# Optimization experiments

Measured on AMD Instinct MI355X. Metric: run time of the kernel, lower is better.

## Reference

```python
import jax, jax.numpy as jnp
import numpy as np

T, M, L, NL, NH, FF = 4096, 512, 128, 2, 8, 2048
NI, NO = 256, 32

def _ln(x, g, b, eps=1e-5):
    mu = x.mean(-1, keepdims=True)
    var = ((x - mu) ** 2).mean(-1, keepdims=True)
    return (x - mu) * jax.lax.rsqrt(var + eps) * g + b

def _mha(x, Wqkv, bqkv, Wo, bo, nh):
    t, m = x.shape
    hd = m // nh
    qkv = x @ Wqkv.T + bqkv  # (T, 3M)
    q, k, v = jnp.split(qkv, 3, axis=-1)
    q = q.reshape(t, nh, hd).transpose(1, 0, 2)
    k = k.reshape(t, nh, hd).transpose(1, 0, 2)
    v = v.reshape(t, nh, hd).transpose(1, 0, 2)
    scores = jnp.einsum('htd,hsd->hts', q, k) / jnp.sqrt(jnp.float32(hd))
    attn = jax.nn.softmax(scores, axis=-1)
    o = jnp.einsum('hts,hsd->htd', attn, v).transpose(1, 0, 2).reshape(t, m)
    return o @ Wo.T + bo

def _seg_softmax(a, seg, n):
    m = jax.lax.stop_gradient(jax.ops.segment_max(a, seg, num_segments=n))
    e = jnp.exp(a - m[seg])
    s = jax.ops.segment_sum(e, seg, num_segments=n)
    return e / s[seg]

def _conv1d(x, K, b, pad):
    y = jax.lax.conv_general_dilated(x, K, (1,), [pad], dimension_numbers=('NCH', 'OIH', 'NCH'))
    return y + b[None, :, None]

def _bn_eval(x, g, b, eps=1e-5):
    # eval-mode BatchNorm1d, running_mean=0, running_var=1
    scale = g * jax.lax.rsqrt(jnp.float32(1.0) + eps)
    if x.ndim == 3:
        return x * scale[None, :, None] + b[None, :, None]
    return x * scale + b

def setup_inputs() -> dict:
    key = jax.random.key(0)
    ks = iter(jax.random.split(key, 64))
    r = lambda shape: jax.random.normal(next(ks), shape, jnp.float32) * 0.02
    datas = jax.random.normal(next(ks), (T, M), jnp.float32)
    Seq_ids = jnp.repeat(jnp.arange(NI, dtype=jnp.int32), T // NI)  # sorted inner-bag ids
    ids = Seq_ids // (NI // NO)  # outer-bag id per instance
    d = dict(datas=datas, Seq_ids=Seq_ids, ids=ids, n_inner=NI, n_outer=NO, n_head=NH)
    d.update(Wqkv=r((NL, 3 * M, M)), bqkv=jnp.zeros((NL, 3 * M)), Wo=r((NL, M, M)), bo=jnp.zeros((NL, M)),
             ln1_g=jnp.ones((NL, M)), ln1_b=jnp.zeros((NL, M)),
             W1=r((NL, FF, M)), b1=jnp.zeros((NL, FF)), W2=r((NL, M, FF)), b2=jnp.zeros((NL, M)),
             ln2_g=jnp.ones((NL, M)), ln2_b=jnp.zeros((NL, M)),
             Wv1=r((L, M)), bv1=jnp.zeros(L), Wu1=r((L, M)), bu1=jnp.zeros(L), Ww1=r((1, L)), bw1=jnp.zeros(1),
             Wv2=r((L, M)), bv2=jnp.zeros(L), Wu2=r((L, M)), bu2=jnp.zeros(L), Ww2=r((1, L)), bw2=jnp.zeros(1),
             Kc1=r((128, 1, 4)), bc1=jnp.zeros(128), gc1=jnp.ones(128), bb1=jnp.zeros(128),
             Kc2=r((128, 128, 5)), bc2=jnp.zeros(128), gc2=jnp.ones(128), bb2=jnp.zeros(128),
             Kc3=r((128, 128, 7)), bc3=jnp.zeros(128), gc3=jnp.ones(128), bb3=jnp.zeros(128),
             Wf1=r((256, 128 * (M // 4))), bf1=jnp.zeros(256), g4=jnp.ones(256), b4=jnp.zeros(256),
             Wf2=r((128, 256)), bf2=jnp.zeros(128), g5=jnp.ones(128), b5=jnp.zeros(128),
             Wf3=r((1, 128)), bf3=jnp.zeros(1))
    return d

def reference(datas, Seq_ids, ids, n_inner, n_outer, n_head, Wqkv, bqkv, Wo, bo, ln1_g, ln1_b, W1, b1, W2, b2, ln2_g, ln2_b, Wv1, bv1, Wu1, bu1, Ww1, bw1, Wv2, bv2, Wu2, bu2, Ww2, bw2, Kc1, bc1, gc1, bb1, Kc2, bc2, gc2, bb2, Kc3, bc3, gc3, bb3, Wf1, bf1, g4, b4, Wf2, bf2, g5, b5, Wf3, bf3):
    h = datas
    for l in range(Wqkv.shape[0]):  # post-norm torch TransformerEncoderLayer, dropout off (eval)
        h = _ln(h + _mha(h, Wqkv[l], bqkv[l], Wo[l], bo[l], n_head), ln1_g[l], ln1_b[l])
        ff = jax.nn.relu(h @ W1[l].T + b1[l]) @ W2[l].T + b2[l]
        h = _ln(h + ff, ln2_g[l], ln2_b[l])
    # level-1 gated attention pooling over inner bags (flat segment form)
    A1 = ((jnp.tanh(h @ Wv1.T + bv1) * jax.nn.sigmoid(h @ Wu1.T + bu1)) @ Ww1.T + bw1)[:, 0]
    w1 = _seg_softmax(A1, Seq_ids, n_inner)
    out1 = jax.ops.segment_sum(w1[:, None] * h, Seq_ids, num_segments=n_inner)  # (NI, M)
    super_ids = jax.ops.segment_min(ids, Seq_ids, num_segments=n_inner)  # first id per inner bag
    # level-2 gated attention pooling over outer bags
    A2 = ((jnp.tanh(out1 @ Wv2.T + bv2) * jax.nn.sigmoid(out1 @ Wu2.T + bu2)) @ Ww2.T + bw2)[:, 0]
    w2 = _seg_softmax(A2, super_ids, n_outer)
    out2 = jax.ops.segment_sum(w2[:, None] * out1, super_ids, num_segments=n_outer)  # (NO, M)
    x = out2[:, None, :]  # (NO, 1, M)
    hc = jax.nn.relu(_bn_eval(_conv1d(x, Kc1, bc1, (1, 2)), gc1, bb1))
    hc = jax.nn.relu(_bn_eval(_conv1d(hc, Kc2, bc2, (2, 2)), gc2, bb2))
    hc = hc.reshape(hc.shape[0], hc.shape[1], -1, 2).mean(-1)  # AvgPool1d(2)
    hc = jax.nn.relu(_bn_eval(_conv1d(hc, Kc3, bc3, (3, 3)), gc3, bb3))
    hc = hc.reshape(hc.shape[0], hc.shape[1], -1, 2).mean(-1)
    hc = hc.reshape(hc.shape[0], -1)  # (NO, 128*(M//4))
    hc = _bn_eval(jax.nn.relu(hc @ Wf1.T + bf1), g4, b4)
    hc = _bn_eval(jax.nn.relu(hc @ Wf2.T + bf2), g5, b5)
    Y_prob = jax.nn.sigmoid(hc @ Wf3.T + bf3)
    Y_hat = (Y_prob >= 0.5).astype(jnp.float32)
    return Y_prob, Y_hat, w1, w2
```

## Files before the change

kernel.cpp:

```cpp
#include <hip/hip_runtime.h>
#include <math.h>


typedef float f32x4 __attribute__((ext_vector_type(4)));
typedef __bf16 bf16x8 __attribute__((ext_vector_type(8)));

__device__ __forceinline__ unsigned short f2bf(float x) {
  unsigned int u = __builtin_bit_cast(unsigned int, x);
  u += 0x7FFFu + ((u >> 16) & 1u);
  return (unsigned short)(u >> 16);
}
__device__ __forceinline__ float bf2f(unsigned short u) {
  unsigned int x = ((unsigned int)u) << 16;
  return __builtin_bit_cast(float, x);
}
__device__ __forceinline__ unsigned int pk_bf16(float a, float b) {
  unsigned int r;
  asm("v_cvt_pk_bf16_f32 %0, %1, %2" : "=v"(r) : "v"(a), "v"(b));
  return r;
}

__device__ __forceinline__ float wave_sum64(float v) {
#pragma unroll
  for (int o = 32; o > 0; o >>= 1) v += __shfl_xor(v, o);
  return v;
}

__device__ __forceinline__ int swz(int byte) {
  return byte ^ (((byte >> 7) & 7) << 4);
}
__device__ __forceinline__ int swz256(int byte) {
  return byte ^ (((byte >> 8) & 7) << 4);
}

template<int ACT, int OUTBF, int VSPLIT>
__global__ __launch_bounds__(256) void mgemm(
    const unsigned short* __restrict__ A, const unsigned short* __restrict__ B,
    const float* __restrict__ bias, float* __restrict__ Cf,
    unsigned short* __restrict__ Cb, unsigned short* __restrict__ VT,
    int M, int N, int K)
{
  __shared__ __align__(16) unsigned short As[128 * 64];
  __shared__ __align__(16) unsigned short Bs[128 * 64];
  const int tid = threadIdx.x;
  const int wid = tid >> 6, lane = tid & 63;
  const int wm = wid >> 1, wn = wid & 1;
  const int l15 = lane & 15, l4 = lane >> 4;
  const int m0 = blockIdx.y * 128, n0 = blockIdx.x * 128;
  const int srow = tid >> 3;
  const int scol = (tid & 7) * 8;

  f32x4 acc[4][4] = {};

  bf16x8 ra[4], rb[4];
#pragma unroll
  for (int i = 0; i < 4; i++) {
    ra[i] = *(const bf16x8*)&A[(size_t)(m0 + srow + i * 32) * K + scol];
    rb[i] = *(const bf16x8*)&B[(size_t)(n0 + srow + i * 32) * K + scol];
  }

  for (int k0 = 0; k0 < K; k0 += 64) {
    __syncthreads();
#pragma unroll
    for (int i = 0; i < 4; i++) {
      int byte = (srow + i * 32) * 128 + scol * 2;
      *(bf16x8*)((char*)As + swz(byte)) = ra[i];
      *(bf16x8*)((char*)Bs + swz(byte)) = rb[i];
    }
    __syncthreads();
    if (k0 + 64 < K) {
#pragma unroll
      for (int i = 0; i < 4; i++) {
        ra[i] = *(const bf16x8*)&A[(size_t)(m0 + srow + i * 32) * K + k0 + 64 + scol];
        rb[i] = *(const bf16x8*)&B[(size_t)(n0 + srow + i * 32) * K + k0 + 64 + scol];
      }
    }
#pragma unroll
    for (int kc = 0; kc < 2; kc++) {
      bf16x8 af[4], bf_[4];
#pragma unroll
      for (int i = 0; i < 4; i++) {
        int byteA = (wm * 64 + i * 16 + l15) * 128 + kc * 64 + l4 * 16;
        af[i] = *(const bf16x8*)((const char*)As + swz(byteA));
        int byteB = (wn * 64 + i * 16 + l15) * 128 + kc * 64 + l4 * 16;
        bf_[i] = *(const bf16x8*)((const char*)Bs + swz(byteB));
      }
#pragma unroll
      for (int i = 0; i < 4; i++)
#pragma unroll
        for (int j = 0; j < 4; j++)
          acc[i][j] = __builtin_amdgcn_mfma_f32_16x16x32_bf16(af[i], bf_[j], acc[i][j], 0, 0, 0);
    }
  }
#pragma unroll
  for (int i = 0; i < 4; i++) {
#pragma unroll
    for (int j = 0; j < 4; j++) {
      int col = n0 + wn * 64 + j * 16 + l15;
      float bv = bias[col];
      if (VSPLIT && col >= 1024) {
        float x0 = acc[i][j][0] + bv, x1 = acc[i][j][1] + bv;
        float x2 = acc[i][j][2] + bv, x3 = acc[i][j][3] + bv;
        uint2 pv;
        pv.x = pk_bf16(x0, x1);
        pv.y = pk_bf16(x2, x3);
        int row0 = m0 + wm * 64 + i * 16 + l4 * 4;
        *(uint2*)&VT[(size_t)(col - 1024) * 4096 + row0] = pv;
      } else {
#pragma unroll
        for (int r = 0; r < 4; r++) {
          int row = m0 + wm * 64 + i * 16 + l4 * 4 + r;
          float x = acc[i][j][r] + bv;
          if (ACT == 1) x = fmaxf(x, 0.f);
          if (ACT == 2) x = tanhf(x);
          if (ACT == 3) x = 1.f / (1.f + expf(-x));
          if (ACT == 4) x = (col < 128) ? tanhf(x) : (1.f / (1.f + expf(-x)));
          if (OUTBF) Cb[(size_t)row * N + col] = f2bf(x);
          else       Cf[(size_t)row * N + col] = x;
        }
      }
    }
  }
}

__global__ __launch_bounds__(256) void attn_mfma(
    const unsigned short* __restrict__ qkv, const unsigned short* __restrict__ VT,
    unsigned short* __restrict__ O)
{
  __shared__ __align__(16) unsigned short Ks[64 * 64];
  __shared__ __align__(16) unsigned short VTs[64 * 64];
  __shared__ __align__(16) unsigned short Ps[64 * 64];
  const int tid = threadIdx.x;
  const int w = tid >> 6, lane = tid & 63;
  const int l15 = lane & 15, l4 = lane >> 4;
  const int h = blockIdx.y, qt = blockIdx.x;
  const float C = 0.18033688011112042f;

  bf16x8 qf[2];
#pragma unroll
  for (int kc = 0; kc < 2; kc++)
    qf[kc] = *(const bf16x8*)&qkv[(size_t)(qt * 64 + w * 16 + l15) * 1536 + h * 64 + kc * 32 + l4 * 8];

  f32x4 oaccT[4] = {};
  float m = -1e30f, l = 0.f;

  const int sr = tid >> 3;
  const int sc = (tid & 7) * 8;
  const int vd = tid >> 2;
  const int vk0 = (tid & 3) * 16;

  const unsigned short* kp0 = qkv + (size_t)sr * 1536 + 512 + h * 64 + sc;
  const unsigned short* kp1 = kp0 + 32 * 1536;
  const unsigned short* vp = VT + (size_t)(h * 64 + vd) * 4096 + vk0;

  bf16x8 rk0 = *(const bf16x8*)kp0;
  bf16x8 rk1 = *(const bf16x8*)kp1;
  bf16x8 rv0 = *(const bf16x8*)vp;
  bf16x8 rv1 = *(const bf16x8*)(vp + 8);

  for (int kt = 0; kt < 64; kt++) {
    __syncthreads();
    {
      int b0 = sr * 128 + sc * 2;
      *(bf16x8*)((char*)Ks + swz(b0)) = rk0;
      int b1 = (sr + 32) * 128 + sc * 2;
      *(bf16x8*)((char*)Ks + swz(b1)) = rk1;
      int vb0 = vd * 128 + vk0 * 2;
      *(bf16x8*)((char*)VTs + swz(vb0)) = rv0;
      *(bf16x8*)((char*)VTs + swz(vb0 + 16)) = rv1;
    }
    __syncthreads();
    if (kt < 63) {
      kp0 += 64 * 1536; kp1 += 64 * 1536; vp += 64;
      rk0 = *(const bf16x8*)kp0;
      rk1 = *(const bf16x8*)kp1;
      rv0 = *(const bf16x8*)vp;
      rv1 = *(const bf16x8*)(vp + 8);
    }

    f32x4 st[4] = {};
    __builtin_amdgcn_s_setprio(1);
#pragma unroll
    for (int kc = 0; kc < 2; kc++) {
#pragma unroll
      for (int nb = 0; nb < 4; nb++) {
        int byte = (nb * 16 + l15) * 128 + kc * 64 + l4 * 16;
        bf16x8 kf = *(const bf16x8*)((const char*)Ks + swz(byte));
        st[nb] = __builtin_amdgcn_mfma_f32_16x16x32_bf16(kf, qf[kc], st[nb], 0, 0, 0);
      }
    }
    __builtin_amdgcn_s_setprio(0);

    float tm = -1e30f;
#pragma unroll
    for (int nb = 0; nb < 4; nb++)
#pragma unroll
      for (int r = 0; r < 4; r++) tm = fmaxf(tm, st[nb][r]);
    tm = fmaxf(tm, __shfl_xor(tm, 16));
    tm = fmaxf(tm, __shfl_xor(tm, 32));
    float mn = fmaxf(m, tm);
    float alpha = exp2f((m - mn) * C);
    float e[4][4];
    float ps = 0.f;
#pragma unroll
    for (int nb = 0; nb < 4; nb++)
#pragma unroll
      for (int r = 0; r < 4; r++) {
        e[nb][r] = exp2f((st[nb][r] - mn) * C);
        ps += e[nb][r];
      }
    ps += __shfl_xor(ps, 16);
    ps += __shfl_xor(ps, 32);
    l = l * alpha + ps;
    m = mn;
#pragma unroll
    for (int nb = 0; nb < 4; nb++) oaccT[nb] *= alpha;

#pragma unroll
    for (int nb = 0; nb < 4; nb++) {
      uint2 pr;
      pr.x = pk_bf16(e[nb][0], e[nb][1]);
      pr.y = pk_bf16(e[nb][2], e[nb][3]);
      int byte = (w * 16 + l15) * 128 + (nb * 16 + l4 * 4) * 2;
      *(uint2*)((char*)Ps + swz(byte)) = pr;
    }

#pragma unroll
    for (int kc = 0; kc < 2; kc++) {
      int bp = (w * 16 + l15) * 128 + kc * 64 + l4 * 16;
      bf16x8 pb = *(const bf16x8*)((const char*)Ps + swz(bp));
      __builtin_amdgcn_s_setprio(1);
#pragma unroll
      for (int nb = 0; nb < 4; nb++) {
        int bv = (nb * 16 + l15) * 128 + kc * 64 + l4 * 16;
        bf16x8 vf = *(const bf16x8*)((const char*)VTs + swz(bv));
        oaccT[nb] = __builtin_amdgcn_mfma_f32_16x16x32_bf16(vf, pb, oaccT[nb], 0, 0, 0);
      }
      __builtin_amdgcn_s_setprio(0);
    }
  }

  float linv = 1.f / l;
  int row = qt * 64 + w * 16 + l15;
#pragma unroll
  for (int nb = 0; nb < 4; nb++) {
    uint2 ov;
    ov.x = pk_bf16(oaccT[nb][0] * linv, oaccT[nb][1] * linv);
    ov.y = pk_bf16(oaccT[nb][2] * linv, oaccT[nb][3] * linv);
    int col = h * 64 + nb * 16 + l4 * 4;
    *(uint2*)&O[(size_t)row * 512 + col] = ov;
  }
}

template<int ACT>
__global__ __launch_bounds__(256) void gemm_bias(
    const float* __restrict__ A, const float* __restrict__ B,
    const float* __restrict__ bias, float* __restrict__ C,
    int M, int N, int K)
{
  __shared__ float As[16][68];
  __shared__ float Bs[16][68];
  const int tid = threadIdx.x;
  const int tx = tid & 15, ty = tid >> 4;
  const int m0 = blockIdx.y * 64, n0 = blockIdx.x * 64;
  const int lr = tid >> 2;
  const int lk = (tid & 3) * 4;
  float acc[4][4] = {};
  for (int k0 = 0; k0 < K; k0 += 16) {
    __syncthreads();
    float4 av = *(const float4*)&A[(size_t)(m0 + lr) * K + k0 + lk];
    float4 bv = *(const float4*)&B[(size_t)(n0 + lr) * K + k0 + lk];
    As[lk + 0][lr] = av.x; As[lk + 1][lr] = av.y; As[lk + 2][lr] = av.z; As[lk + 3][lr] = av.w;
    Bs[lk + 0][lr] = bv.x; Bs[lk + 1][lr] = bv.y; Bs[lk + 2][lr] = bv.z; Bs[lk + 3][lr] = bv.w;
    __syncthreads();
#pragma unroll
    for (int k = 0; k < 16; k++) {
      float a[4], b[4];
#pragma unroll
      for (int i = 0; i < 4; i++) a[i] = As[k][ty * 4 + i];
#pragma unroll
      for (int j = 0; j < 4; j++) b[j] = Bs[k][tx * 4 + j];
#pragma unroll
      for (int i = 0; i < 4; i++)
#pragma unroll
        for (int j = 0; j < 4; j++)
          acc[i][j] = fmaf(a[i], b[j], acc[i][j]);
    }
  }
#pragma unroll
  for (int i = 0; i < 4; i++)
#pragma unroll
    for (int j = 0; j < 4; j++) {
      float x = acc[i][j] + bias[n0 + tx * 4 + j];
      if (ACT == 1) x = fmaxf(x, 0.f);
      if (ACT == 2) x = tanhf(x);
      if (ACT == 3) x = 1.f / (1.f + expf(-x));
      C[(size_t)(m0 + ty * 4 + i) * N + n0 + tx * 4 + j] = x;
    }
}

__global__ __launch_bounds__(64) void residual_ln(
    const float* __restrict__ x, const float* __restrict__ res,
    const float* __restrict__ g, const float* __restrict__ b,
    float* __restrict__ out, unsigned short* __restrict__ out_bf)
{
  const int row = blockIdx.x, lane = threadIdx.x;
  const float* xp = x + (size_t)row * 512;
  const float* rp = res + (size_t)row * 512;
  float v[8];
  float s = 0.f;
#pragma unroll
  for (int i = 0; i < 8; i++) { v[i] = xp[lane + 64 * i] + rp[lane + 64 * i]; s += v[i]; }
  s = wave_sum64(s);
  float mu = s * (1.f / 512.f);
  float vs = 0.f;
#pragma unroll
  for (int i = 0; i < 8; i++) { float d = v[i] - mu; vs = fmaf(d, d, vs); }
  vs = wave_sum64(vs);
  float rstd = rsqrtf(vs * (1.f / 512.f) + 1e-5f);
  float* op = out + (size_t)row * 512;
  unsigned short* ob = out_bf + (size_t)row * 512;
#pragma unroll
  for (int i = 0; i < 8; i++) {
    float y = (v[i] - mu) * rstd * g[lane + 64 * i] + b[lane + 64 * i];
    op[lane + 64 * i] = y;
    ob[lane + 64 * i] = f2bf(y);
  }
}

struct CastJobs {
  const float* src[6];
  unsigned short* dst[6];
  int n4[6];
  int njobs;
};

__global__ void cast_multi(CastJobs J)
{
  for (int j = 0; j < J.njobs; j++) {
    const float4* s = (const float4*)J.src[j];
    ushort4* d = (ushort4*)J.dst[j];
    int n = J.n4[j];
    for (int i = blockIdx.x * 256 + threadIdx.x; i < n; i += gridDim.x * 256) {
      float4 v = s[i];
      ushort4 u;
      u.x = f2bf(v.x); u.y = f2bf(v.y); u.z = f2bf(v.z); u.w = f2bf(v.w);
      d[i] = u;
    }
  }
}

__global__ void init_h(const float* __restrict__ in, float* __restrict__ hf,
                       unsigned short* __restrict__ hb, int n4)
{
  int i = blockIdx.x * 256 + threadIdx.x;
  if (i < n4) {
    float4 v = ((const float4*)in)[i];
    ((float4*)hf)[i] = v;
    ushort4 u;
    u.x = f2bf(v.x); u.y = f2bf(v.y); u.z = f2bf(v.z); u.w = f2bf(v.w);
    ((ushort4*)hb)[i] = u;
  }
}

__global__ __launch_bounds__(128) void gate_dot(
    const float* __restrict__ Gv, const float* __restrict__ Gu, int ld,
    const float* __restrict__ Ww, const float* __restrict__ bw,
    float* __restrict__ A)
{
  const int t = blockIdx.x, l = threadIdx.x;
  float v = Gv[(size_t)t * ld + l] * Gu[(size_t)t * ld + l] * Ww[l];
  v = wave_sum64(v);
  __shared__ float red[2];
  if ((l & 63) == 0) red[l >> 6] = v;
  __syncthreads();
  if (l == 0) A[t] = red[0] + red[1] + bw[0];
}

__global__ __launch_bounds__(256) void seg_pool(
    const float* __restrict__ A, const float* __restrict__ X,
    float* __restrict__ w_out, float* __restrict__ out, int seg_len)
{
  const int s = blockIdx.x, tid = threadIdx.x;
  __shared__ float ws[16];
  if (tid < 64) {
    float a = (tid < seg_len) ? A[s * seg_len + tid] : -1e30f;
    float mx = a;
#pragma unroll
    for (int o = 1; o < 16; o <<= 1) mx = fmaxf(mx, __shfl_xor(mx, o));
    float e = (tid < seg_len) ? expf(a - mx) : 0.f;
    float se = e;
#pragma unroll
    for (int o = 1; o < 16; o <<= 1) se += __shfl_xor(se, o);
    if (tid < seg_len) {
      float w = e / se;
      ws[tid] = w;
      w_out[s * seg_len + tid] = w;
    }
  }
  __syncthreads();
  for (int d = tid; d < 512; d += 256) {
    float acc = 0.f;
    for (int i = 0; i < seg_len; i++)
      acc = fmaf(ws[i], X[(size_t)(s * seg_len + i) * 512 + d], acc);
    out[(size_t)s * 512 + d] = acc;
  }
}


__global__ void conv1_bnT(
    const float* __restrict__ x, const float* __restrict__ K4,
    const float* __restrict__ bias, const float* __restrict__ g,
    const float* __restrict__ bb, unsigned short* __restrict__ y)
{
  int idx = blockIdx.x * 256 + threadIdx.x;
  int o = idx & 127, i = (idx >> 7) & 511, n = idx >> 16;
  const float* xp = x + n * 512;
  float acc = bias[o];
#pragma unroll
  for (int k = 0; k < 4; k++) {
    int p = i + k - 1;
    float xv = (p >= 0 && p < 512) ? xp[p] : 0.f;
    acc = fmaf(xv, K4[o * 4 + k], acc);
  }
  float sc = g[o] * rsqrtf(1.f + 1e-5f);
  y[idx] = f2bf(fmaxf(fmaf(acc, sc, bb[o]), 0.f));
}

__global__ void reorder_w(const float* __restrict__ Kc, unsigned short* __restrict__ Wr,
                          int KS, int total)
{
  int idx = blockIdx.x * 256 + threadIdx.x;
  if (idx < total) {
    int c = idx & 127;
    int kk = (idx >> 7) % KS;
    int o = idx / (128 * KS);
    Wr[idx] = f2bf(Kc[(o * 128 + c) * KS + kk]);
  }
}

template<int KS, int PAD, int LEN, int OUTF>
__global__ __launch_bounds__(256) void convT_mfma(
    const unsigned short* __restrict__ X, const unsigned short* __restrict__ Wr,
    const float* __restrict__ bias, const float* __restrict__ g,
    const float* __restrict__ bb,
    unsigned short* __restrict__ Yb, float* __restrict__ Yf)
{
  constexpr int ROWS = 64 + KS - 1;
  __shared__ __align__(16) unsigned short XT[ROWS * 128];
  const int tid = threadIdx.x;
  const int w = tid >> 6, lane = tid & 63;
  const int l15 = lane & 15, l4 = lane >> 4;
  const int i0 = (blockIdx.x >> 1) * 64;
  const int o0 = (blockIdx.x & 1) * 64;
  const int n = blockIdx.y;

  {
    const int c = (tid & 15) * 8;
    for (int r = tid >> 4; r < ROWS; r += 16) {
      int gi = i0 - PAD + r;
      bf16x8 v = {};
      if (gi >= 0 && gi < LEN)
        v = *(const bf16x8*)&X[((size_t)n * LEN + gi) * 128 + c];
      int byte = r * 256 + c * 2;
      *(bf16x8*)((char*)XT + swz256(byte)) = v;
    }
  }
  __syncthreads();

  f32x4 acc[4] = {};
#pragma unroll
  for (int kk = 0; kk < KS; kk++) {
#pragma unroll
    for (int cc = 0; cc < 4; cc++) {
      int r = w * 16 + l15 + kk;
      int byte = r * 256 + cc * 64 + l4 * 16;
      bf16x8 a = *(const bf16x8*)((const char*)XT + swz256(byte));
      bf16x8 bfr[4];
#pragma unroll
      for (int nb = 0; nb < 4; nb++)
        bfr[nb] = *(const bf16x8*)&Wr[(size_t)(o0 + nb * 16 + l15) * (KS * 128) +
                                      kk * 128 + cc * 32 + l4 * 8];
#pragma unroll
      for (int nb = 0; nb < 4; nb++)
        acc[nb] = __builtin_amdgcn_mfma_f32_16x16x32_bf16(a, bfr[nb], acc[nb], 0, 0, 0);
    }
  }

#pragma unroll
  for (int nb = 0; nb < 4; nb++) {
    int o = o0 + nb * 16 + l15;
    float sc = g[o] * rsqrtf(1.f + 1e-5f);
    float bs = bias[o], bo_ = bb[o];
#pragma unroll
    for (int rr = 0; rr < 4; rr++) {
      int i = i0 + w * 16 + l4 * 4 + rr;
      float v = fmaxf(fmaf(acc[nb][rr] + bs, sc, bo_), 0.f);
      size_t oidx = ((size_t)n * LEN + i) * 128 + o;
      if (OUTF) Yf[oidx] = v;
      else Yb[oidx] = f2bf(v);
    }
  }
}

__global__ void avgpool2_bf(const unsigned short* __restrict__ x,
                            unsigned short* __restrict__ y, int nI, int nTot4)
{
  int j = blockIdx.x * 256 + threadIdx.x;
  if (j >= nTot4) return;
  int cq = j & 31;
  int i = (j >> 5) % nI;
  int n = j / (nI * 32);
  const ushort4* a = (const ushort4*)&x[(((size_t)n * nI + i) * 2) * 128 + cq * 4];
  const ushort4* b = (const ushort4*)&x[(((size_t)n * nI + i) * 2 + 1) * 128 + cq * 4];
  ushort4 ua = *a, ub = *b;
  ushort4 r;
  r.x = f2bf(0.5f * (bf2f(ua.x) + bf2f(ub.x)));
  r.y = f2bf(0.5f * (bf2f(ua.y) + bf2f(ub.y)));
  r.z = f2bf(0.5f * (bf2f(ua.z) + bf2f(ub.z)));
  r.w = f2bf(0.5f * (bf2f(ua.w) + bf2f(ub.w)));
  ((ushort4*)y)[j] = r;
}

__global__ void pool3_transpose(const float* __restrict__ x, float* __restrict__ y)
{
  int j = blockIdx.x * 256 + threadIdx.x;
  if (j >= 524288) return;
  int i = j & 127, c = (j >> 7) & 127, n = j >> 14;
  const float* b = x + ((size_t)n * 256 + 2 * i) * 128 + c;
  y[j] = 0.5f * (b[0] + b[128]);
}

__global__ __launch_bounds__(256) void fc1_kernel(
    const float* __restrict__ x, const float* __restrict__ W,
    const float* __restrict__ bias, const float* __restrict__ g,
    const float* __restrict__ bb, float* __restrict__ y)
{
  int o = blockIdx.x & 255, n = blockIdx.x >> 8;
  const float* xp = x + (size_t)n * 16384;
  const float* wp = W + (size_t)o * 16384;
  float s = 0.f;
  for (int j = threadIdx.x * 4; j < 16384; j += 1024) {
    float4 a = *(const float4*)(xp + j);
    float4 b = *(const float4*)(wp + j);
    s = fmaf(a.x, b.x, s); s = fmaf(a.y, b.y, s);
    s = fmaf(a.z, b.z, s); s = fmaf(a.w, b.w, s);
  }
  s = wave_sum64(s);
  __shared__ float red[4];
  if ((threadIdx.x & 63) == 0) red[threadIdx.x >> 6] = s;
  __syncthreads();
  if (threadIdx.x == 0) {
    float v = red[0] + red[1] + red[2] + red[3] + bias[o];
    v = fmaxf(v, 0.f);
    y[n * 256 + o] = fmaf(v, g[o] * rsqrtf(1.f + 1e-5f), bb[o]);
  }
}

__global__ __launch_bounds__(256) void fc2_kernel(
    const float* __restrict__ x, const float* __restrict__ W,
    const float* __restrict__ bias, const float* __restrict__ g,
    const float* __restrict__ bb, float* __restrict__ y)
{
  int o = blockIdx.x & 127, n = blockIdx.x >> 7;
  float s = x[n * 256 + threadIdx.x] * W[o * 256 + threadIdx.x];
  s = wave_sum64(s);
  __shared__ float red[4];
  if ((threadIdx.x & 63) == 0) red[threadIdx.x >> 6] = s;
  __syncthreads();
  if (threadIdx.x == 0) {
    float v = red[0] + red[1] + red[2] + red[3] + bias[o];
    v = fmaxf(v, 0.f);
    y[n * 128 + o] = fmaf(v, g[o] * rsqrtf(1.f + 1e-5f), bb[o]);
  }
}

__global__ __launch_bounds__(64) void fc3_kernel(
    const float* __restrict__ x, const float* __restrict__ W,
    const float* __restrict__ bias, float* __restrict__ out)
{
  int n = threadIdx.x;
  if (n < 32) {
    float s = bias[0];
    for (int k = 0; k < 128; k++) s = fmaf(x[n * 128 + k], W[k], s);
    float p = 1.f / (1.f + expf(-s));
    out[n] = p;
    out[32 + n] = (p >= 0.5f) ? 1.f : 0.f;
  }
}

extern "C" void kernel_launch(void* const* d_in, const int* in_sizes, int n_in,
                              void* d_out, int out_size, void* d_ws, size_t ws_size,
                              hipStream_t stream)
{
  const float* datas = (const float*)d_in[0];
  const float* Wqkv = (const float*)d_in[6];
  const float* bqkv = (const float*)d_in[7];
  const float* Wo   = (const float*)d_in[8];
  const float* bo   = (const float*)d_in[9];
  const float* ln1g = (const float*)d_in[10];
  const float* ln1b = (const float*)d_in[11];
  const float* W1   = (const float*)d_in[12];
  const float* b1   = (const float*)d_in[13];
  const float* W2   = (const float*)d_in[14];
  const float* b2   = (const float*)d_in[15];
  const float* ln2g = (const float*)d_in[16];
  const float* ln2b = (const float*)d_in[17];
  const float* Wv1  = (const float*)d_in[18];
  const float* bv1  = (const float*)d_in[19];
  const float* Wu1  = (const float*)d_in[20];
  const float* bu1  = (const float*)d_in[21];
  const float* Ww1  = (const float*)d_in[22];
  const float* bw1  = (const float*)d_in[23];
  const float* Wv2  = (const float*)d_in[24];
  const float* bv2  = (const float*)d_in[25];
  const float* Wu2  = (const float*)d_in[26];
  const float* bu2  = (const float*)d_in[27];
  const float* Ww2  = (const float*)d_in[28];
  const float* bw2  = (const float*)d_in[29];
  const float* Kc1  = (const float*)d_in[30];
  const float* bc1  = (const float*)d_in[31];
  const float* gc1  = (const float*)d_in[32];
  const float* bb1  = (const float*)d_in[33];
  const float* Kc2  = (const float*)d_in[34];
  const float* bc2  = (const float*)d_in[35];
  const float* gc2  = (const float*)d_in[36];
  const float* bb2  = (const float*)d_in[37];
  const float* Kc3  = (const float*)d_in[38];
  const float* bc3  = (const float*)d_in[39];
  const float* gc3  = (const float*)d_in[40];
  const float* bb3  = (const float*)d_in[41];
  const float* Wf1  = (const float*)d_in[42];
  const float* bf1  = (const float*)d_in[43];
  const float* g4   = (const float*)d_in[44];
  const float* b4   = (const float*)d_in[45];
  const float* Wf2  = (const float*)d_in[46];
  const float* bf2  = (const float*)d_in[47];
  const float* g5   = (const float*)d_in[48];
  const float* b5   = (const float*)d_in[49];
  const float* Wf3  = (const float*)d_in[50];
  const float* bf3  = (const float*)d_in[51];

  float* ws = (float*)d_ws;
  float* h_f32 = ws;
  float* R2f   = ws + 2097152;
  unsigned short* h_bf = (unsigned short*)(ws + 8388608);
  unsigned short* wbuf = (unsigned short*)(ws + 9437184);
  float* biasG = ws + 11173888;
  unsigned short* VTg = (unsigned short*)(ws + 11174144);

  unsigned short* qkv_bf = (unsigned short*)R2f;
  unsigned short* O_bf   = (unsigned short*)(R2f + 3145728);
  unsigned short* ff1_bf = (unsigned short*)R2f;
  float* projf = R2f + 4194304;

  unsigned short* WqkvB = wbuf;
  unsigned short* WoB   = wbuf + 786432;
  unsigned short* W1B   = wbuf + 1048576;
  unsigned short* W2B   = wbuf + 2097152;
  unsigned short* WvuB  = wbuf + 3145728;
  unsigned short* Wr2B  = wbuf + 3276800;
  unsigned short* Wr3B  = wbuf + 3358720;

  float* out_f = (float*)d_out;

  init_h<<<2048, 256, 0, stream>>>(datas, h_f32, h_bf, 524288);
  reorder_w<<<320, 256, 0, stream>>>(Kc2, Wr2B, 5, 81920);
  reorder_w<<<448, 256, 0, stream>>>(Kc3, Wr3B, 7, 114688);
  hipMemcpyAsync(biasG, bv1, 128 * sizeof(float), hipMemcpyDeviceToDevice, stream);
  hipMemcpyAsync(biasG + 128, bu1, 128 * sizeof(float), hipMemcpyDeviceToDevice, stream);

  for (int l = 0; l < 2; l++) {
    CastJobs J{};
    J.src[0] = Wqkv + (size_t)l * 786432;  J.dst[0] = WqkvB; J.n4[0] = 196608;
    J.src[1] = Wo   + (size_t)l * 262144;  J.dst[1] = WoB;   J.n4[1] = 65536;
    J.src[2] = W1   + (size_t)l * 1048576; J.dst[2] = W1B;   J.n4[2] = 262144;
    J.src[3] = W2   + (size_t)l * 1048576; J.dst[3] = W2B;   J.n4[3] = 262144;
    J.njobs = 4;
    if (l == 0) {
      J.src[4] = Wv1; J.dst[4] = WvuB;         J.n4[4] = 16384;
      J.src[5] = Wu1; J.dst[5] = WvuB + 65536; J.n4[5] = 16384;
      J.njobs = 6;
    }
    cast_multi<<<512, 256, 0, stream>>>(J);

    mgemm<0, 1, 1><<<dim3(12, 32), 256, 0, stream>>>(
        h_bf, WqkvB, bqkv + (size_t)l * 1536, nullptr, qkv_bf, VTg, 4096, 1536, 512);
    attn_mfma<<<dim3(64, 8), 256, 0, stream>>>(qkv_bf, VTg, O_bf);
    mgemm<0, 0, 0><<<dim3(4, 32), 256, 0, stream>>>(
        O_bf, WoB, bo + (size_t)l * 512, projf, nullptr, nullptr, 4096, 512, 512);
    residual_ln<<<4096, 64, 0, stream>>>(projf, h_f32, ln1g + l * 512, ln1b + l * 512,
                                         h_f32, h_bf);
    mgemm<1, 1, 0><<<dim3(16, 32), 256, 0, stream>>>(
        h_bf, W1B, b1 + (size_t)l * 2048, nullptr, ff1_bf, nullptr, 4096, 2048, 512);
    mgemm<0, 0, 0><<<dim3(4, 32), 256, 0, stream>>>(
        ff1_bf, W2B, b2 + (size_t)l * 512, projf, nullptr, nullptr, 4096, 512, 2048);
    residual_ln<<<4096, 64, 0, stream>>>(projf, h_f32, ln2g + l * 512, ln2b + l * 512,
                                         h_f32, h_bf);
  }

  float* G    = R2f;
  float* A1   = R2f + 1048576;
  float* out1 = R2f + 1052672;
  float* Gv2  = R2f + 1183744;
  float* Gu2  = R2f + 1216512;
  float* A2   = R2f + 1249280;
  float* out2 = R2f + 1249536;

  mgemm<4, 0, 0><<<dim3(2, 32), 256, 0, stream>>>(
      h_bf, WvuB, biasG, G, nullptr, nullptr, 4096, 256, 512);
  gate_dot<<<4096, 128, 0, stream>>>(G, G + 128, 256, Ww1, bw1, A1);
  seg_pool<<<256, 256, 0, stream>>>(A1, h_f32, out_f + 64, out1, 16);

  gemm_bias<2><<<dim3(2, 4), 256, 0, stream>>>(out1, Wv2, bv2, Gv2, 256, 128, 512);
  gemm_bias<3><<<dim3(2, 4), 256, 0, stream>>>(out1, Wu2, bu2, Gu2, 256, 128, 512);
  gate_dot<<<256, 128, 0, stream>>>(Gv2, Gu2, 128, Ww2, bw2, A2);
  seg_pool<<<32, 256, 0, stream>>>(A2, out1, out_f + 4160, out2, 8);

  unsigned short* c1T = (unsigned short*)(R2f + 1310720);
  unsigned short* c2T = (unsigned short*)(R2f + 2359296);
  unsigned short* p2T = (unsigned short*)(R2f + 3407872);
  float* c3T = R2f + 3932160;
  float* p3R = R2f + 4980736;
  float* f1  = R2f + 5505024;
  float* f2  = R2f + 5513216;

  conv1_bnT<<<8192, 256, 0, stream>>>(out2, Kc1, bc1, gc1, bb1, c1T);
  convT_mfma<5, 2, 512, 0><<<dim3(16, 32), 256, 0, stream>>>(
      c1T, Wr2B, bc2, gc2, bb2, c2T, nullptr);
  avgpool2_bf<<<1024, 256, 0, stream>>>(c2T, p2T, 256, 262144);
  convT_mfma<7, 3, 256, 1><<<dim3(8, 32), 256, 0, stream>>>(
      p2T, Wr3B, bc3, gc3, bb3, nullptr, c3T);
  pool3_transpose<<<2048, 256, 0, stream>>>(c3T, p3R);
  fc1_kernel<<<8192, 256, 0, stream>>>(p3R, Wf1, bf1, g4, b4, f1);
  fc2_kernel<<<4096, 256, 0, stream>>>(f1, Wf2, bf2, g5, b5, f2);
  fc3_kernel<<<1, 64, 0, stream>>>(f2, Wf3, bf3, out_f);
}
```

Baseline: 608.5 us.

## Process two 64-query sub-tiles per attention block to reuse K/V tiles

Each attention block now handles 128 query rows as two independent 64-row sub-tiles. Both share each K and V tile staged in shared memory, and the grid is halved accordingly. This halves global and LDS traffic for K/V per query and doubles MFMA work per synchronization. In exchange it raises register use and halves the number of blocks, which may reduce occupancy and parallelism across CUs.

```diff
diff --git a/kernel.cpp b/kernel.cpp
--- a/kernel.cpp
+++ b/kernel.cpp
@@ -129,20 +129,23 @@
 {
   __shared__ __align__(16) unsigned short Ks[64 * 64];
   __shared__ __align__(16) unsigned short VTs[64 * 64];
-  __shared__ __align__(16) unsigned short Ps[64 * 64];
+  __shared__ __align__(16) unsigned short Ps[128 * 64];
   const int tid = threadIdx.x;
   const int w = tid >> 6, lane = tid & 63;
   const int l15 = lane & 15, l4 = lane >> 4;
   const int h = blockIdx.y, qt = blockIdx.x;
   const float C = 0.18033688011112042f;
 
-  bf16x8 qf[2];
-#pragma unroll
-  for (int kc = 0; kc < 2; kc++)
-    qf[kc] = *(const bf16x8*)&qkv[(size_t)(qt * 64 + w * 16 + l15) * 1536 + h * 64 + kc * 32 + l4 * 8];
-
-  f32x4 oaccT[4] = {};
-  float m = -1e30f, l = 0.f;
+  bf16x8 qf[2][2];
+#pragma unroll
+  for (int s = 0; s < 2; s++)
+#pragma unroll
+    for (int kc = 0; kc < 2; kc++)
+      qf[s][kc] = *(const bf16x8*)&qkv[(size_t)(qt * 128 + s * 64 + w * 16 + l15) * 1536 +
+                                       h * 64 + kc * 32 + l4 * 8];
+
+  f32x4 oaccT[2][4] = {};
+  float m[2] = {-1e30f, -1e30f}, l[2] = {0.f, 0.f};
 
   const int sr = tid >> 3;
   const int sc = (tid & 7) * 8;
@@ -178,7 +181,7 @@
       rv1 = *(const bf16x8*)(vp + 8);
     }
 
-    f32x4 st[4] = {};
+    f32x4 st[2][4] = {};
     __builtin_amdgcn_s_setprio(1);
 #pragma unroll
     for (int kc = 0; kc < 2; kc++) {
@@ -186,69 +189,79 @@
       for (int nb = 0; nb < 4; nb++) {
         int byte = (nb * 16 + l15) * 128 + kc * 64 + l4 * 16;
         bf16x8 kf = *(const bf16x8*)((const char*)Ks + swz(byte));
-        st[nb] = __builtin_amdgcn_mfma_f32_16x16x32_bf16(kf, qf[kc], st[nb], 0, 0, 0);
+        st[0][nb] = __builtin_amdgcn_mfma_f32_16x16x32_bf16(kf, qf[0][kc], st[0][nb], 0, 0, 0);
+        st[1][nb] = __builtin_amdgcn_mfma_f32_16x16x32_bf16(kf, qf[1][kc], st[1][nb], 0, 0, 0);
       }
     }
     __builtin_amdgcn_s_setprio(0);
 
-    float tm = -1e30f;
-#pragma unroll
-    for (int nb = 0; nb < 4; nb++)
-#pragma unroll
-      for (int r = 0; r < 4; r++) tm = fmaxf(tm, st[nb][r]);
-    tm = fmaxf(tm, __shfl_xor(tm, 16));
-    tm = fmaxf(tm, __shfl_xor(tm, 32));
-    float mn = fmaxf(m, tm);
-    float alpha = exp2f((m - mn) * C);
-    float e[4][4];
-    float ps = 0.f;
-#pragma unroll
-    for (int nb = 0; nb < 4; nb++)
-#pragma unroll
-      for (int r = 0; r < 4; r++) {
-        e[nb][r] = exp2f((st[nb][r] - mn) * C);
-        ps += e[nb][r];
+#pragma unroll
+    for (int s = 0; s < 2; s++) {
+      float tm = -1e30f;
+#pragma unroll
+      for (int nb = 0; nb < 4; nb++)
+#pragma unroll
+        for (int r = 0; r < 4; r++) tm = fmaxf(tm, st[s][nb][r]);
+      tm = fmaxf(tm, __shfl_xor(tm, 16));
+      tm = fmaxf(tm, __shfl_xor(tm, 32));
+      float mn = fmaxf(m[s], tm);
+      float alpha = exp2f((m[s] - mn) * C);
+      float e[4][4];
+      float ps = 0.f;
+#pragma unroll
+      for (int nb = 0; nb < 4; nb++)
+#pragma unroll
+        for (int r = 0; r < 4; r++) {
+          e[nb][r] = exp2f((st[s][nb][r] - mn) * C);
+          ps += e[nb][r];
+        }
+      ps += __shfl_xor(ps, 16);
+      ps += __shfl_xor(ps, 32);
+      l[s] = l[s] * alpha + ps;
+      m[s] = mn;
+#pragma unroll
+      for (int nb = 0; nb < 4; nb++) oaccT[s][nb] *= alpha;
+
+#pragma unroll
+      for (int nb = 0; nb < 4; nb++) {
+        uint2 pr;
+        pr.x = pk_bf16(e[nb][0], e[nb][1]);
+        pr.y = pk_bf16(e[nb][2], e[nb][3]);
+        int byte = (s * 64 + w * 16 + l15) * 128 + (nb * 16 + l4 * 4) * 2;
+        *(uint2*)((char*)Ps + swz(byte)) = pr;
       }
-    ps += __shfl_xor(ps, 16);
-    ps += __shfl_xor(ps, 32);
-    l = l * alpha + ps;
-    m = mn;
-#pragma unroll
-    for (int nb = 0; nb < 4; nb++) oaccT[nb] *= alpha;
-
-#pragma unroll
-    for (int nb = 0; nb < 4; nb++) {
-      uint2 pr;
-      pr.x = pk_bf16(e[nb][0], e[nb][1]);
-      pr.y = pk_bf16(e[nb][2], e[nb][3]);
-      int byte = (w * 16 + l15) * 128 + (nb * 16 + l4 * 4) * 2;
-      *(uint2*)((char*)Ps + swz(byte)) = pr;
     }
 
 #pragma unroll
     for (int kc = 0; kc < 2; kc++) {
-      int bp = (w * 16 + l15) * 128 + kc * 64 + l4 * 16;
-      bf16x8 pb = *(const bf16x8*)((const char*)Ps + swz(bp));
+      int bp0 = (w * 16 + l15) * 128 + kc * 64 + l4 * 16;
+      bf16x8 pb0 = *(const bf16x8*)((const char*)Ps + swz(bp0));
+      int bp1 = (64 + w * 16 + l15) * 128 + kc * 64 + l4 * 16;
+      bf16x8 pb1 = *(const bf16x8*)((const char*)Ps + swz(bp1));
       __builtin_amdgcn_s_setprio(1);
 #pragma unroll
       for (int nb = 0; nb < 4; nb++) {
         int bv = (nb * 16 + l15) * 128 + kc * 64 + l4 * 16;
         bf16x8 vf = *(const bf16x8*)((const char*)VTs + swz(bv));
-        oaccT[nb] = __builtin_amdgcn_mfma_f32_16x16x32_bf16(vf, pb, oaccT[nb], 0, 0, 0);
+        oaccT[0][nb] = __builtin_amdgcn_mfma_f32_16x16x32_bf16(vf, pb0, oaccT[0][nb], 0, 0, 0);
+        oaccT[1][nb] = __builtin_amdgcn_mfma_f32_16x16x32_bf16(vf, pb1, oaccT[1][nb], 0, 0, 0);
       }
       __builtin_amdgcn_s_setprio(0);
     }
   }
 
-  float linv = 1.f / l;
-  int row = qt * 64 + w * 16 + l15;
-#pragma unroll
-  for (int nb = 0; nb < 4; nb++) {
-    uint2 ov;
-    ov.x = pk_bf16(oaccT[nb][0] * linv, oaccT[nb][1] * linv);
-    ov.y = pk_bf16(oaccT[nb][2] * linv, oaccT[nb][3] * linv);
-    int col = h * 64 + nb * 16 + l4 * 4;
-    *(uint2*)&O[(size_t)row * 512 + col] = ov;
+#pragma unroll
+  for (int s = 0; s < 2; s++) {
+    float linv = 1.f / l[s];
+    int row = qt * 128 + s * 64 + w * 16 + l15;
+#pragma unroll
+    for (int nb = 0; nb < 4; nb++) {
+      uint2 ov;
+      ov.x = pk_bf16(oaccT[s][nb][0] * linv, oaccT[s][nb][1] * linv);
+      ov.y = pk_bf16(oaccT[s][nb][2] * linv, oaccT[s][nb][3] * linv);
+      int col = h * 64 + nb * 16 + l4 * 4;
+      *(uint2*)&O[(size_t)row * 512 + col] = ov;
+    }
   }
 }
 
@@ -686,7 +699,7 @@
 
     mgemm<0, 1, 1><<<dim3(12, 32), 256, 0, stream>>>(
         h_bf, WqkvB, bqkv + (size_t)l * 1536, nullptr, qkv_bf, VTg, 4096, 1536, 512);
-    attn_mfma<<<dim3(64, 8), 256, 0, stream>>>(qkv_bf, VTg, O_bf);
+    attn_mfma<<<dim3(32, 8), 256, 0, stream>>>(qkv_bf, VTg, O_bf);
     mgemm<0, 0, 0><<<dim3(4, 32), 256, 0, stream>>>(
         O_bf, WoB, bo + (size_t)l * 512, projf, nullptr, nullptr, 4096, 512, 512);
     residual_ln<<<4096, 64, 0, stream>>>(projf, h_f32, ln1g + l * 512, ln1b + l * 512,
```

Result: slower. 664.0 us (+9.1%).

## Load GEMM tiles straight into LDS with global_load_lds, dropping register staging

Applied to the files above, without the earlier changes.

The bf16 GEMM now fills its shared-memory A/B tiles with direct global-to-LDS 16-byte loads, replacing the register-staged copy and LDS stores. This removes the VGPR staging and the store instructions. It also drops the XOR swizzle on the LDS layout, which can bring back bank conflicts on the fragment reads. It removes the register prefetch of the next K tile as well, so global loads no longer overlap the MFMA work of the current tile.

```diff
diff --git a/kernel.cpp b/kernel.cpp
--- a/kernel.cpp
+++ b/kernel.cpp
@@ -18,6 +18,13 @@
   unsigned int r;
   asm("v_cvt_pk_bf16_f32 %0, %1, %2" : "=v"(r) : "v"(a), "v"(b));
   return r;
+}
+
+__device__ __forceinline__ void gload16(const unsigned short* g, unsigned short* l) {
+  __builtin_amdgcn_global_load_lds(
+      (const __attribute__((address_space(1))) unsigned int*)(uintptr_t)g,
+      (__attribute__((address_space(3))) unsigned int*)(unsigned int)(uintptr_t)l,
+      16, 0, 0);
 }
 
 __device__ __forceinline__ float wave_sum64(float v) {
@@ -40,50 +47,37 @@
     unsigned short* __restrict__ Cb, unsigned short* __restrict__ VT,
     int M, int N, int K)
 {
-  __shared__ __align__(16) unsigned short As[128 * 64];
-  __shared__ __align__(16) unsigned short Bs[128 * 64];
+  __shared__ __align__(1024) unsigned short As[128 * 64];
+  __shared__ __align__(1024) unsigned short Bs[128 * 64];
   const int tid = threadIdx.x;
   const int wid = tid >> 6, lane = tid & 63;
   const int wm = wid >> 1, wn = wid & 1;
   const int l15 = lane & 15, l4 = lane >> 4;
   const int m0 = blockIdx.y * 128, n0 = blockIdx.x * 128;
-  const int srow = tid >> 3;
-  const int scol = (tid & 7) * 8;
+  const int srow8 = lane >> 3;
+  const int scol  = (lane & 7) * 8;
 
   f32x4 acc[4][4] = {};
-
-  bf16x8 ra[4], rb[4];
-#pragma unroll
-  for (int i = 0; i < 4; i++) {
-    ra[i] = *(const bf16x8*)&A[(size_t)(m0 + srow + i * 32) * K + scol];
-    rb[i] = *(const bf16x8*)&B[(size_t)(n0 + srow + i * 32) * K + scol];
-  }
 
   for (int k0 = 0; k0 < K; k0 += 64) {
     __syncthreads();
 #pragma unroll
-    for (int i = 0; i < 4; i++) {
-      int byte = (srow + i * 32) * 128 + scol * 2;
-      *(bf16x8*)((char*)As + swz(byte)) = ra[i];
-      *(bf16x8*)((char*)Bs + swz(byte)) = rb[i];
+    for (int t = 0; t < 4; t++) {
+      int chunk = wid * 4 + t;
+      int row = chunk * 8 + srow8;
+      gload16(&A[(size_t)(m0 + row) * K + k0 + scol], &As[chunk * 512]);
+      gload16(&B[(size_t)(n0 + row) * K + k0 + scol], &Bs[chunk * 512]);
     }
     __syncthreads();
-    if (k0 + 64 < K) {
-#pragma unroll
-      for (int i = 0; i < 4; i++) {
-        ra[i] = *(const bf16x8*)&A[(size_t)(m0 + srow + i * 32) * K + k0 + 64 + scol];
-        rb[i] = *(const bf16x8*)&B[(size_t)(n0 + srow + i * 32) * K + k0 + 64 + scol];
-      }
-    }
 #pragma unroll
     for (int kc = 0; kc < 2; kc++) {
       bf16x8 af[4], bf_[4];
 #pragma unroll
       for (int i = 0; i < 4; i++) {
         int byteA = (wm * 64 + i * 16 + l15) * 128 + kc * 64 + l4 * 16;
-        af[i] = *(const bf16x8*)((const char*)As + swz(byteA));
+        af[i] = *(const bf16x8*)((const char*)As + byteA);
         int byteB = (wn * 64 + i * 16 + l15) * 128 + kc * 64 + l4 * 16;
-        bf_[i] = *(const bf16x8*)((const char*)Bs + swz(byteB));
+        bf_[i] = *(const bf16x8*)((const char*)Bs + byteB);
       }
 #pragma unroll
       for (int i = 0; i < 4; i++)
```

Result: slower. 650.2 us (+6.9%).

## Replace fc1 scalar dot-product kernel with split-K bf16 MFMA plus reduction

Applied to the files above, without the earlier changes.

The first fully connected layer (32x16384 by 256x16384) moves from one block per output doing fp32 dot products to a split-K bf16 MFMA kernel over 64 K-groups, followed by a small reduction kernel that applies bias, ReLU and BN. The pooled activations are written as bf16 and Wf1 is cast to bf16 into a reused workspace region on every call. Each weight element is now read once instead of once per batch row, which cuts memory traffic. In exchange it adds a cast pass over the 16M-element weight, precision loss from bf16, and a partial-sum buffer round trip.

```diff
diff --git a/kernel.cpp b/kernel.cpp
--- a/kernel.cpp
+++ b/kernel.cpp
@@ -522,39 +522,63 @@
   ((ushort4*)y)[j] = r;
 }
 
-__global__ void pool3_transpose(const float* __restrict__ x, float* __restrict__ y)
+__global__ void pool3_transpose_bf(const float* __restrict__ x,
+                                   unsigned short* __restrict__ y)
 {
   int j = blockIdx.x * 256 + threadIdx.x;
   if (j >= 524288) return;
   int i = j & 127, c = (j >> 7) & 127, n = j >> 14;
   const float* b = x + ((size_t)n * 256 + 2 * i) * 128 + c;
-  y[j] = 0.5f * (b[0] + b[128]);
-}
-
-__global__ __launch_bounds__(256) void fc1_kernel(
-    const float* __restrict__ x, const float* __restrict__ W,
-    const float* __restrict__ bias, const float* __restrict__ g,
-    const float* __restrict__ bb, float* __restrict__ y)
-{
-  int o = blockIdx.x & 255, n = blockIdx.x >> 8;
-  const float* xp = x + (size_t)n * 16384;
-  const float* wp = W + (size_t)o * 16384;
+  y[j] = f2bf(0.5f * (b[0] + b[128]));
+}
+
+__global__ __launch_bounds__(256) void fc1_mfma(
+    const unsigned short* __restrict__ X, const unsigned short* __restrict__ WB,
+    float* __restrict__ pt)
+{
+  const int tid = threadIdx.x;
+  const int w = tid >> 6, lane = tid & 63;
+  const int l15 = lane & 15, l4 = lane >> 4;
+  const int ot = blockIdx.x & 1;
+  const int kg = blockIdx.x >> 1;
+  const int k0 = kg * 256;
+
+  f32x4 acc[2][2] = {};
+  for (int kk = 0; kk < 256; kk += 32) {
+    bf16x8 a0 = *(const bf16x8*)&X[(size_t)l15 * 16384 + k0 + kk + l4 * 8];
+    bf16x8 a1 = *(const bf16x8*)&X[(size_t)(16 + l15) * 16384 + k0 + kk + l4 * 8];
+#pragma unroll
+    for (int nb = 0; nb < 2; nb++) {
+      int o = ot * 128 + w * 32 + nb * 16 + l15;
+      bf16x8 b = *(const bf16x8*)&WB[(size_t)o * 16384 + k0 + kk + l4 * 8];
+      acc[0][nb] = __builtin_amdgcn_mfma_f32_16x16x32_bf16(a0, b, acc[0][nb], 0, 0, 0);
+      acc[1][nb] = __builtin_amdgcn_mfma_f32_16x16x32_bf16(a1, b, acc[1][nb], 0, 0, 0);
+    }
+  }
+#pragma unroll
+  for (int mf = 0; mf < 2; mf++)
+#pragma unroll
+    for (int nb = 0; nb < 2; nb++) {
+      int o = ot * 128 + w * 32 + nb * 16 + l15;
+#pragma unroll
+      for (int r = 0; r < 4; r++) {
+        int n = mf * 16 + l4 * 4 + r;
+        pt[((size_t)kg * 32 + n) * 256 + o] = acc[mf][nb][r];
+      }
+    }
+}
+
+__global__ __launch_bounds__(256) void fc1_reduce(
+    const float* __restrict__ pt, const float* __restrict__ bias,
+    const float* __restrict__ g, const float* __restrict__ bb,
+    float* __restrict__ y)
+{
+  int o = threadIdx.x, n = blockIdx.x;
   float s = 0.f;
-  for (int j = threadIdx.x * 4; j < 16384; j += 1024) {
-    float4 a = *(const float4*)(xp + j);
-    float4 b = *(const float4*)(wp + j);
-    s = fmaf(a.x, b.x, s); s = fmaf(a.y, b.y, s);
-    s = fmaf(a.z, b.z, s); s = fmaf(a.w, b.w, s);
-  }
-  s = wave_sum64(s);
-  __shared__ float red[4];
-  if ((threadIdx.x & 63) == 0) red[threadIdx.x >> 6] = s;
-  __syncthreads();
-  if (threadIdx.x == 0) {
-    float v = red[0] + red[1] + red[2] + red[3] + bias[o];
-    v = fmaxf(v, 0.f);
-    y[n * 256 + o] = fmaf(v, g[o] * rsqrtf(1.f + 1e-5f), bb[o]);
-  }
+  for (int kg = 0; kg < 64; kg++) s += pt[((size_t)kg * 32 + n) * 256 + o];
+  s += bias[o];
+  s = fmaxf(s, 0.f);
+  y[n * 256 + o] = fmaf(s, g[o] * rsqrtf(1.f + 1e-5f), bb[o]);
 }
 
 __global__ __launch_bounds__(256) void fc2_kernel(
@@ -662,6 +686,8 @@
   unsigned short* Wr2B  = wbuf + 3276800;
   unsigned short* Wr3B  = wbuf + 3358720;
 
+  unsigned short* Wf1B = (unsigned short*)h_f32;
+
   float* out_f = (float*)d_out;
 
   init_h<<<2048, 256, 0, stream>>>(datas, h_f32, h_bf, 524288);
@@ -712,6 +738,13 @@
   gate_dot<<<4096, 128, 0, stream>>>(G, G + 128, 256, Ww1, bw1, A1);
   seg_pool<<<256, 256, 0, stream>>>(A1, h_f32, out_f + 64, out1, 16);
 
+  {
+    CastJobs J{};
+    J.src[0] = Wf1; J.dst[0] = Wf1B; J.n4[0] = 1048576;
+    J.njobs = 1;
+    cast_multi<<<512, 256, 0, stream>>>(J);
+  }
+
   gemm_bias<2><<<dim3(2, 4), 256, 0, stream>>>(out1, Wv2, bv2, Gv2, 256, 128, 512);
   gemm_bias<3><<<dim3(2, 4), 256, 0, stream>>>(out1, Wu2, bu2, Gu2, 256, 128, 512);
   gate_dot<<<256, 128, 0, stream>>>(Gv2, Gu2, 128, Ww2, bw2, A2);
@@ -721,9 +754,10 @@
   unsigned short* c2T = (unsigned short*)(R2f + 2359296);
   unsigned short* p2T = (unsigned short*)(R2f + 3407872);
   float* c3T = R2f + 3932160;
-  float* p3R = R2f + 4980736;
-  float* f1  = R2f + 5505024;
-  float* f2  = R2f + 5513216;
+  unsigned short* p3B = (unsigned short*)(R2f + 4980736);
+  float* pt  = R2f + 5242880;
+  float* f1  = R2f + 5767168;
+  float* f2  = R2f + 5775360;
 
   conv1_bnT<<<8192, 256, 0, stream>>>(out2, Kc1, bc1, gc1, bb1, c1T);
   convT_mfma<5, 2, 512, 0><<<dim3(16, 32), 256, 0, stream>>>(
@@ -731,8 +765,9 @@
   avgpool2_bf<<<1024, 256, 0, stream>>>(c2T, p2T, 256, 262144);
   convT_mfma<7, 3, 256, 1><<<dim3(8, 32), 256, 0, stream>>>(
       p2T, Wr3B, bc3, gc3, bb3, nullptr, c3T);
-  pool3_transpose<<<2048, 256, 0, stream>>>(c3T, p3R);
-  fc1_kernel<<<8192, 256, 0, stream>>>(p3R, Wf1, bf1, g4, b4, f1);
+  pool3_transpose_bf<<<2048, 256, 0, stream>>>(c3T, p3B);
+  fc1_mfma<<<128, 256, 0, stream>>>(p3B, Wf1B, pt);
+  fc1_reduce<<<32, 256, 0, stream>>>(pt, bf1, g4, b4, f1);
   fc2_kernel<<<4096, 256, 0, stream>>>(f1, Wf2, bf2, g5, b5, f2);
   fc3_kernel<<<1, 64, 0, stream>>>(f2, Wf3, bf3, out_f);
 }
```

Measured after the change: 594.8 us. -2.3%, faster.
